# Kernel tuning notes

Measured on AMD Instinct MI355X. Metric: run time of the kernel, lower is better.

Reference implementation:

```python
import jax, jax.numpy as jnp
import numpy as np

B, C, D, H, W = 1, 128, 8, 32, 32
NH, HD = 8, 16            # num_heads, head_dim = C // NH
PD, PH, PW = 2, 4, 4      # local patch dims
RD, RH, RW = 2, 2, 2      # global K/V reduction ratios
MLPH = 4 * C              # mlp_ratio = 4
EPS = 1e-5
SCALE = HD ** -0.5


def setup_inputs() -> dict:
    key = jax.random.key(0)
    ks = iter(jax.random.split(key, 16))
    def w(shape, scale=0.02):
        return jax.random.normal(next(ks), shape, jnp.float32) * scale
    inp = {"x": jax.random.normal(next(ks), (B, C, D, H, W), jnp.float32)}
    for p in ("l", "g"):  # local branch / global branch transformer blocks
        inp[f"{p}_n1_g"] = jnp.ones((C,), jnp.float32)
        inp[f"{p}_n1_b"] = jnp.zeros((C,), jnp.float32)
        inp[f"{p}_qkv_w"] = w((3 * C, C))            # Linear(dim, 3*dim, bias=False)
        inp[f"{p}_proj_w"] = w((C, C))
        inp[f"{p}_proj_b"] = jnp.zeros((C,), jnp.float32)
        inp[f"{p}_n2_g"] = jnp.ones((C,), jnp.float32)
        inp[f"{p}_n2_b"] = jnp.zeros((C,), jnp.float32)
        inp[f"{p}_fc1_w"] = w((MLPH, C))
        inp[f"{p}_fc1_b"] = jnp.zeros((MLPH,), jnp.float32)
        inp[f"{p}_fc2_w"] = w((C, MLPH))
        inp[f"{p}_fc2_b"] = jnp.zeros((C,), jnp.float32)
    inp["g_ke_w"] = w((C, C, RD, RH, RW))  # Conv3d(dim, dim, k=stride=(2,2,2), bias=False)
    inp["g_ve_w"] = w((C, C, RD, RH, RW))
    inp["g_nk_g"] = jnp.ones((HD,), jnp.float32)
    inp["g_nk_b"] = jnp.zeros((HD,), jnp.float32)
    inp["g_nv_g"] = jnp.ones((HD,), jnp.float32)
    inp["g_nv_b"] = jnp.zeros((HD,), jnp.float32)
    return inp


def _ln(t, g, b):
    m = t.mean(-1, keepdims=True)
    v = jnp.square(t - m).mean(-1, keepdims=True)
    return (t - m) * jax.lax.rsqrt(v + EPS) * g + b


def _mlp(t, w1, b1, w2, b2):
    return jax.nn.gelu(t @ w1.T + b1, approximate=False) @ w2.T + b2


def _forward(x, l_n1_g, l_n1_b, l_qkv_w, l_proj_w, l_proj_b, l_n2_g, l_n2_b,
             l_fc1_w, l_fc1_b, l_fc2_w, l_fc2_b,
             g_n1_g, g_n1_b, g_qkv_w, g_ke_w, g_ve_w, g_nk_g, g_nk_b,
             g_nv_g, g_nv_b, g_proj_w, g_proj_b, g_n2_g, g_n2_b,
             g_fc1_w, g_fc1_b, g_fc2_w, g_fc2_b):
    nd, nh, nw = D // PD, H // PH, W // PW
    R, Npl = nd * nh * nw, PD * PH * PW
    N = D * H * W

    # ---------------- Local branch ----------------
    # (B,C,D,H,W) -> (B, R, Npl, C) patch tokens
    loc = x.reshape(B, C, nd, PD, nh, PH, nw, PW)
    loc = loc.transpose(0, 2, 4, 6, 3, 5, 7, 1).reshape(B, R, Npl, C)
    y = _ln(loc, l_n1_g, l_n1_b)
    qkv = (y @ l_qkv_w.T).reshape(B, R, Npl, 3, NH, HD).transpose(3, 0, 1, 4, 2, 5)
    q, k, v = qkv[0], qkv[1], qkv[2]  # (B,R,NH,Npl,HD)
    attn = jax.nn.softmax(jnp.einsum('brhnd,brhmd->brhnm', q, k) * SCALE, axis=-1)
    o = jnp.einsum('brhnm,brhmd->brhnd', attn, v)
    # faithful to torch: (attn@v).transpose(-1,-2).reshape(B,R,Npl,C)
    o = jnp.swapaxes(o, -1, -2).reshape(B, R, Npl, C)
    loc = loc + (o @ l_proj_w.T + l_proj_b)
    loc = loc + _mlp(_ln(loc, l_n2_g, l_n2_b), l_fc1_w, l_fc1_b, l_fc2_w, l_fc2_b)
    # back to (B,C,D,H,W)
    loc_y = loc.reshape(B, nd, nh, nw, PD, PH, PW, C)
    loc_y = loc_y.transpose(0, 7, 1, 4, 2, 5, 3, 6).reshape(B, C, D, H, W)

    # ---------------- Global branch ----------------
    g = x.reshape(B, C, N).transpose(0, 2, 1)  # (B,N,C)
    y = _ln(g, g_n1_g, g_n1_b)
    qkv = y @ g_qkv_w.T  # (B,N,3C)
    q, k, v = jnp.split(qkv, 3, axis=-1)
    qh = q.reshape(B, N, NH, HD).transpose(0, 2, 1, 3)  # (B,NH,N,HD)
    dn = ('NCDHW', 'OIDHW', 'NCDHW')
    def _reduce(t, wc):
        tm = t.transpose(0, 2, 1).reshape(B, C, D, H, W)
        tr = jax.lax.conv_general_dilated(tm, wc, (RD, RH, RW), 'VALID',
                                          dimension_numbers=dn)
        nr = tr.shape[2] * tr.shape[3] * tr.shape[4]
        return tr.reshape(B, C, nr).transpose(0, 2, 1).reshape(B, nr, NH, HD).transpose(0, 2, 1, 3)
    kr = _ln(_reduce(k, g_ke_w), g_nk_g, g_nk_b)  # (B,NH,Nr,HD)
    vr = _ln(_reduce(v, g_ve_w), g_nv_g, g_nv_b)
    attn = jax.nn.softmax(jnp.einsum('bhnd,bhmd->bhnm', qh, kr) * SCALE, axis=-1)
    o = jnp.einsum('bhnm,bhmd->bhnd', attn, vr)
    o = o.transpose(0, 2, 1, 3).reshape(B, N, C)
    g = g + (o @ g_proj_w.T + g_proj_b)
    g = g + _mlp(_ln(g, g_n2_g, g_n2_b), g_fc1_w, g_fc1_b, g_fc2_w, g_fc2_b)
    glo_y = g.transpose(0, 2, 1).reshape(B, C, D, H, W)

    # ---------------- Gate ----------------
    return x * jax.nn.sigmoid(loc_y + glo_y)


def reference(x, l_n1_g, l_n1_b, l_qkv_w, l_proj_w, l_proj_b, l_n2_g, l_n2_b,
              l_fc1_w, l_fc1_b, l_fc2_w, l_fc2_b,
              g_n1_g, g_n1_b, g_qkv_w, g_ke_w, g_ve_w, g_nk_g, g_nk_b,
              g_nv_g, g_nv_b, g_proj_w, g_proj_b, g_n2_g, g_n2_b,
              g_fc1_w, g_fc1_b, g_fc2_w, g_fc2_b):
    return _forward(x, l_n1_g, l_n1_b, l_qkv_w, l_proj_w, l_proj_b, l_n2_g, l_n2_b,
                    l_fc1_w, l_fc1_b, l_fc2_w, l_fc2_b,
                    g_n1_g, g_n1_b, g_qkv_w, g_ke_w, g_ve_w, g_nk_g, g_nk_b,
                    g_nv_g, g_nv_b, g_proj_w, g_proj_b, g_n2_g, g_n2_b,
                    g_fc1_w, g_fc1_b, g_fc2_w, g_fc2_b)
```

## Files before the change

### kernel.cpp

```cpp
#include <hip/hip_runtime.h>
#include <math.h>

#define N_TOK 8192
#define C_DIM 128
#define NHD   8
#define HDIM  16
#define NR    1024
#define EPSV  1e-5f
#define QK_SCALE 0.25f
#define QK_L2E  0.36067376f

typedef __attribute__((ext_vector_type(8))) short short8;
typedef __attribute__((ext_vector_type(4))) float f32x4;

__device__ __forceinline__ float gelu_f(float v) {
    return 0.5f * v * (1.0f + erff(v * 0.70710678118654752f));
}
__device__ __forceinline__ float uaf(unsigned int u) {
    union { unsigned int u; float f; } x; x.u = u; return x.f;
}
__device__ __forceinline__ short f2b(float v) {
    union { float f; unsigned int u; } x; x.f = v;
    unsigned int r = x.u + 0x7fffu + ((x.u >> 16) & 1u);
    return (short)(r >> 16);
}
__device__ __forceinline__ unsigned int pk2(float a, float b) {
    return (unsigned int)(unsigned short)f2b(a) | ((unsigned int)(unsigned short)f2b(b) << 16);
}
__device__ __forceinline__ void ld16bf(const short* p, float* d) {
    uint4 a = *(const uint4*)p;
    uint4 b = *(const uint4*)(p + 8);
    d[0]  = uaf(a.x << 16); d[1]  = uaf(a.x & 0xffff0000u);
    d[2]  = uaf(a.y << 16); d[3]  = uaf(a.y & 0xffff0000u);
    d[4]  = uaf(a.z << 16); d[5]  = uaf(a.z & 0xffff0000u);
    d[6]  = uaf(a.w << 16); d[7]  = uaf(a.w & 0xffff0000u);
    d[8]  = uaf(b.x << 16); d[9]  = uaf(b.x & 0xffff0000u);
    d[10] = uaf(b.y << 16); d[11] = uaf(b.y & 0xffff0000u);
    d[12] = uaf(b.z << 16); d[13] = uaf(b.z & 0xffff0000u);
    d[14] = uaf(b.w << 16); d[15] = uaf(b.w & 0xffff0000u);
}

struct CvtDesc { const float* src; short* dst; int n; int pad; };
struct CvtArgs { CvtDesc d[10]; };

__global__ __launch_bounds__(256) void prep_k(const float* __restrict__ x,
                                              const float* __restrict__ g1, const float* __restrict__ b1,
                                              const float* __restrict__ g2, const float* __restrict__ b2,
                                              float* __restrict__ xt,
                                              short* __restrict__ o1, short* __restrict__ o2,
                                              CvtArgs ca) {
    __shared__ float tile[32][132];
    int t = threadIdx.x;
    if (blockIdx.x >= 256) {
        int bid = blockIdx.x - 256;
#pragma unroll 1
        for (int d = 0; d < 10; ++d) {
            CvtDesc dd = ca.d[d];
            if (dd.pad) {
                for (int i = bid * 256 + t; i < dd.n; i += 40 * 256) {
                    int co = i >> 10, qq = i & 1023;
                    dd.dst[co * 1024 + ((qq & 7) << 7) + (qq >> 3)] = f2b(dd.src[i]);
                }
            } else {
                for (int i = bid * 256 + t; i < dd.n; i += 40 * 256)
                    dd.dst[i] = f2b(dd.src[i]);
            }
        }
        return;
    }
    int n0 = blockIdx.x * 32;
#pragma unroll
    for (int k = 0; k < 16; ++k) {
        int f = t + k * 256;
        int n = f & 31, c = f >> 5;
        tile[n][c] = x[(size_t)c * N_TOK + n0 + n];
    }
    __syncthreads();
    int tk = t >> 3, cb = (t & 7) * 16;
    float v[16];
    float s = 0.f, sq = 0.f;
#pragma unroll
    for (int i = 0; i < 16; ++i) {
        v[i] = tile[tk][cb + i];
        s += v[i]; sq += v[i] * v[i];
    }
    s += __shfl_xor(s, 1);  s += __shfl_xor(s, 2);  s += __shfl_xor(s, 4);
    sq += __shfl_xor(sq, 1); sq += __shfl_xor(sq, 2); sq += __shfl_xor(sq, 4);
    float m = s * (1.0f / 128.0f);
    float var = sq * (1.0f / 128.0f) - m * m;
    float rs = rsqrtf(var + EPSV);
    int tok = n0 + tk;
    float* xp = xt + (size_t)tok * C_DIM + cb;
    *(float4*)(xp)      = make_float4(v[0], v[1], v[2], v[3]);
    *(float4*)(xp + 4)  = make_float4(v[4], v[5], v[6], v[7]);
    *(float4*)(xp + 8)  = make_float4(v[8], v[9], v[10], v[11]);
    *(float4*)(xp + 12) = make_float4(v[12], v[13], v[14], v[15]);
    float hA[16], hB[16];
#pragma unroll
    for (int i = 0; i < 16; ++i) {
        float hn = (v[i] - m) * rs;
        hA[i] = hn * g1[cb + i] + b1[cb + i];
        hB[i] = hn * g2[cb + i] + b2[cb + i];
    }
    uint4 ua0 = {pk2(hA[0], hA[1]), pk2(hA[2], hA[3]), pk2(hA[4], hA[5]), pk2(hA[6], hA[7])};
    uint4 ua1 = {pk2(hA[8], hA[9]), pk2(hA[10], hA[11]), pk2(hA[12], hA[13]), pk2(hA[14], hA[15])};
    uint4 ub0 = {pk2(hB[0], hB[1]), pk2(hB[2], hB[3]), pk2(hB[4], hB[5]), pk2(hB[6], hB[7])};
    uint4 ub1 = {pk2(hB[8], hB[9]), pk2(hB[10], hB[11]), pk2(hB[12], hB[13]), pk2(hB[14], hB[15])};
    *(uint4*)(o1 + (size_t)tok * C_DIM + cb)     = ua0;
    *(uint4*)(o1 + (size_t)tok * C_DIM + cb + 8) = ua1;
    *(uint4*)(o2 + (size_t)tok * C_DIM + cb)     = ub0;
    *(uint4*)(o2 + (size_t)tok * C_DIM + cb + 8) = ub1;
}

__global__ __launch_bounds__(256) void ln2_pair_k(const float* __restrict__ in0,
                                                  const float* __restrict__ g0, const float* __restrict__ b0,
                                                  short* __restrict__ o0,
                                                  const float* __restrict__ in1,
                                                  const float* __restrict__ g1, const float* __restrict__ b1,
                                                  short* __restrict__ o1) {
    int blk = blockIdx.x;
    bool sel = blk >= 2048;
    blk &= 2047;
    const float* in = sel ? in1 : in0;
    const float* g  = sel ? g1 : g0;
    const float* b  = sel ? b1 : b0;
    short* o        = sel ? o1 : o0;
    int lane = threadIdx.x & 63;
    int n = blk * 4 + (threadIdx.x >> 6);
    float v0 = in[(size_t)n * C_DIM + lane];
    float v1 = in[(size_t)n * C_DIM + 64 + lane];
    float s = v0 + v1, sq = v0 * v0 + v1 * v1;
#pragma unroll
    for (int off = 32; off >= 1; off >>= 1) {
        s += __shfl_xor(s, off);
        sq += __shfl_xor(sq, off);
    }
    float m = s * (1.0f / 128.0f);
    float var = sq * (1.0f / 128.0f) - m * m;
    float rs = rsqrtf(var + EPSV);
    o[(size_t)n * C_DIM + lane]      = f2b((v0 - m) * rs * g[lane] + b[lane]);
    o[(size_t)n * C_DIM + 64 + lane] = f2b((v1 - m) * rs * g[lane + 64] + b[lane + 64]);
}

struct MArgs {
    const short* A[2]; const short* W[2];
    const float* bias[2]; const float* res[2];
    void* out[2];
};
template <int EPI>
__global__ __launch_bounds__(256) void mgemm_k(MArgs ga, int M, int N, int K) {
    int zi = blockIdx.z;
    const short* A = ga.A[zi];
    const short* W = ga.W[zi];
    __shared__ short As[128 * 64];
    __shared__ short Bs[128 * 64];
    int t = threadIdx.x;
    int w = t >> 6, l = t & 63;
    int m0 = blockIdx.x * 128, n0 = blockIdx.y * 128;
    int wm = (w >> 1) * 64, wn = (w & 1) * 64;

    f32x4 acc[4][4];
#pragma unroll
    for (int a = 0; a < 4; ++a)
#pragma unroll
        for (int b = 0; b < 4; ++b) acc[a][b] = f32x4{0.f, 0.f, 0.f, 0.f};

    for (int k0 = 0; k0 < K; k0 += 64) {
        __syncthreads();
#pragma unroll
        for (int c = 0; c < 4; ++c) {
            int chunk = c * 256 + t;
            int row = chunk >> 3;
            int slot = chunk & 7;
            int ss = slot ^ (row & 7);
            uint4 av = *(const uint4*)(A + (size_t)(m0 + row) * K + k0 + slot * 8);
            *(uint4*)(As + row * 64 + ss * 8) = av;
            uint4 wv = *(const uint4*)(W + (size_t)(n0 + row) * K + k0 + slot * 8);
            *(uint4*)(Bs + row * 64 + ss * 8) = wv;
        }
        __syncthreads();
#pragma unroll
        for (int kk = 0; kk < 2; ++kk) {
            short8 af[4], bf[4];
            int sl = kk * 4 + (l >> 4);
#pragma unroll
            for (int mf = 0; mf < 4; ++mf) {
                int row = wm + mf * 16 + (l & 15);
                af[mf] = *(const short8*)(As + row * 64 + (sl ^ (row & 7)) * 8);
            }
#pragma unroll
            for (int nf = 0; nf < 4; ++nf) {
                int row = wn + nf * 16 + (l & 15);
                bf[nf] = *(const short8*)(Bs + row * 64 + (sl ^ (row & 7)) * 8);
            }
#pragma unroll
            for (int mf = 0; mf < 4; ++mf)
#pragma unroll
                for (int nf = 0; nf < 4; ++nf)
                    acc[mf][nf] = __builtin_amdgcn_mfma_f32_16x16x32_bf16(
                        af[mf], bf[nf], acc[mf][nf], 0, 0, 0);
        }
    }

#pragma unroll
    for (int mf = 0; mf < 4; ++mf) {
#pragma unroll
        for (int nf = 0; nf < 4; ++nf) {
            int col = n0 + wn + nf * 16 + (l & 15);
#pragma unroll
            for (int j = 0; j < 4; ++j) {
                int row = m0 + wm + mf * 16 + (l >> 4) * 4 + j;
                float v = acc[mf][nf][j];
                if (EPI == 0) {
                    ((short*)ga.out[zi])[(size_t)row * N + col] = f2b(v);
                } else if (EPI == 1) {
                    v += ga.bias[zi][col] + ga.res[zi][(size_t)row * N + col];
                    ((float*)ga.out[zi])[(size_t)row * N + col] = v;
                } else if (EPI == 2) {
                    v = gelu_f(v + ga.bias[zi][col]);
                    ((short*)ga.out[zi])[(size_t)row * N + col] = f2b(v);
                }
            }
        }
    }
}

struct CLArgs {
    const short* qkv_g; const short* wk; const short* wv;
    float* kpart; float* vpart;
    const short* qkv_l; short* ob;
};
__global__ __launch_bounds__(256) void convlat_k(CLArgs ga) {
    __shared__ char smem[32768];
    int t = threadIdx.x;
    if (blockIdx.x < 128) {
        int bid = blockIdx.x;
        int m0 = (bid & 7) * 128;
        int zi = bid >> 6;
        int slice = (bid >> 3) & 7;
        const short* Abase = ga.qkv_g + (zi ? 256 : 128);
        const short* W = zi ? ga.wv : ga.wk;
        float* outp = zi ? ga.vpart : ga.kpart;
        short* As = (short*)smem;
        short* Bs = (short*)smem + 128 * 64;
        int w = t >> 6, l = t & 63;
        int wm = (w >> 1) * 64, wn = (w & 1) * 64;
        int kbeg = slice * 128;

        f32x4 acc[4][4];
#pragma unroll
        for (int a = 0; a < 4; ++a)
#pragma unroll
            for (int b = 0; b < 4; ++b) acc[a][b] = f32x4{0.f, 0.f, 0.f, 0.f};

        for (int k0 = kbeg; k0 < kbeg + 128; k0 += 64) {
            __syncthreads();
            int off = k0 >> 7;
            int od = off >> 2, oh = (off >> 1) & 1, ow = off & 1;
#pragma unroll
            for (int c = 0; c < 4; ++c) {
                int chunk = c * 256 + t;
                int row = chunk >> 3;
                int slot = chunk & 7;
                int ss = slot ^ (row & 7);
                int nr = m0 + row;
                int ci = (k0 & 127) + slot * 8;
                int n = (2 * (nr >> 8) + od) * 1024 + (2 * ((nr >> 4) & 15) + oh) * 32
                        + 2 * (nr & 15) + ow;
                uint4 av = *(const uint4*)(Abase + (size_t)n * 384 + ci);
                *(uint4*)(As + row * 64 + ss * 8) = av;
                uint4 wv2 = *(const uint4*)(W + (size_t)row * 1024 + k0 + slot * 8);
                *(uint4*)(Bs + row * 64 + ss * 8) = wv2;
            }
            __syncthreads();
#pragma unroll
            for (int kk = 0; kk < 2; ++kk) {
                short8 af[4], bf[4];
                int sl = kk * 4 + (l >> 4);
#pragma unroll
                for (int mf = 0; mf < 4; ++mf) {
                    int row = wm + mf * 16 + (l & 15);
                    af[mf] = *(const short8*)(As + row * 64 + (sl ^ (row & 7)) * 8);
                }
#pragma unroll
                for (int nf = 0; nf < 4; ++nf) {
                    int row = wn + nf * 16 + (l & 15);
                    bf[nf] = *(const short8*)(Bs + row * 64 + (sl ^ (row & 7)) * 8);
                }
#pragma unroll
                for (int mf = 0; mf < 4; ++mf)
#pragma unroll
                    for (int nf = 0; nf < 4; ++nf)
                        acc[mf][nf] = __builtin_amdgcn_mfma_f32_16x16x32_bf16(
                            af[mf], bf[nf], acc[mf][nf], 0, 0, 0);
            }
        }
#pragma unroll
        for (int mf = 0; mf < 4; ++mf)
#pragma unroll
            for (int nf = 0; nf < 4; ++nf) {
                int col = wn + nf * 16 + (l & 15);
#pragma unroll
                for (int j = 0; j < 4; ++j) {
                    int row = m0 + wm + mf * 16 + (l >> 4) * 4 + j;
                    outp[(size_t)slice * (NR * C_DIM) + (size_t)row * C_DIM + col] =
                        acc[mf][nf][j];
                }
            }
        return;
    }
    float (*ks)[32][HDIM] = (float(*)[32][HDIM])smem;
    float (*vs)[32][HDIM] = (float(*)[32][HDIM])(smem + 16384);
    int m = t & 31, h = t >> 5, r = blockIdx.x - 128;
    int zd = r >> 6, zh = (r >> 3) & 7, zw = r & 7;
    int pd = m >> 4, ph = (m >> 2) & 3, pw = m & 3;
    int n = (zd * 2 + pd) * 1024 + (zh * 4 + ph) * 32 + (zw * 4 + pw);
    const short* base = ga.qkv_l + (size_t)n * 384 + h * HDIM;
    float q[16], kt[16], vt[16];
    ld16bf(base, q);
    ld16bf(base + 128, kt);
    ld16bf(base + 256, vt);
#pragma unroll
    for (int d = 0; d < 16; ++d) { ks[h][m][d] = kt[d]; vs[h][m][d] = vt[d]; }
    __syncthreads();
    float s[32];
#pragma unroll
    for (int j = 0; j < 32; ++j) {
        float d = 0.f;
#pragma unroll
        for (int dd = 0; dd < 16; ++dd) d += q[dd] * ks[h][j][dd];
        s[j] = __expf(d * QK_SCALE);
    }
    float sum = 0.f;
#pragma unroll
    for (int j = 0; j < 32; ++j) sum += s[j];
    float inv = 1.0f / sum;
    float oo[16] = {};
#pragma unroll
    for (int j = 0; j < 32; ++j) {
        float p = s[j] * inv;
#pragma unroll
        for (int dd = 0; dd < 16; ++dd) oo[dd] += p * vs[h][j][dd];
    }
#pragma unroll
    for (int dd = 0; dd < 16; ++dd) {
        int n2 = h * 4 + (dd >> 2);
        int c2 = (dd & 3) * 32 + m;
        int pd2 = n2 >> 4, ph2 = (n2 >> 2) & 3, pw2 = n2 & 3;
        int nn = (zd * 2 + pd2) * 1024 + (zh * 4 + ph2) * 32 + (zw * 4 + pw2);
        ga.ob[(size_t)nn * C_DIM + c2] = f2b(oo[dd]);
    }
}

__global__ __launch_bounds__(256) void ln_head_sum_k(const float* __restrict__ kpart,
                                                     const float* __restrict__ vpart,
                                                     const float* __restrict__ gk, const float* __restrict__ bk,
                                                     const float* __restrict__ gv, const float* __restrict__ bv,
                                                     short* __restrict__ kout, short* __restrict__ vout) {
    int idx = blockIdx.x * 256 + threadIdx.x;
    bool sel = idx >= 8192;
    int id2 = idx & 8191;
    const float* part = sel ? vpart : kpart;
    const float* g    = sel ? gv : gk;
    const float* b    = sel ? bv : bk;
    int nr = id2 >> 3, h = id2 & 7;
    size_t base = (size_t)nr * C_DIM + h * HDIM;
    float v[16] = {};
#pragma unroll
    for (int p = 0; p < 8; ++p) {
        const float* pp = part + (size_t)p * (NR * C_DIM) + base;
#pragma unroll
        for (int d4 = 0; d4 < 4; ++d4) {
            float4 t = *(const float4*)(pp + d4 * 4);
            v[d4 * 4 + 0] += t.x; v[d4 * 4 + 1] += t.y;
            v[d4 * 4 + 2] += t.z; v[d4 * 4 + 3] += t.w;
        }
    }
    float s = 0.f;
#pragma unroll
    for (int i = 0; i < 16; ++i) s += v[i];
    float m = s * (1.0f / 16.0f);
    float sq = 0.f;
#pragma unroll
    for (int i = 0; i < 16; ++i) { float d = v[i] - m; sq += d * d; }
    float rs = rsqrtf(sq * (1.0f / 16.0f) + EPSV);
    if (!sel) {
        short* op = kout + (size_t)h * (NR * HDIM) + (size_t)nr * HDIM;
#pragma unroll
        for (int i = 0; i < 16; ++i)
            op[i] = f2b(((v[i] - m) * rs * g[i] + b[i]) * QK_L2E);
    } else {
        short* op = vout + (size_t)h * (HDIM * NR) + nr;
#pragma unroll
        for (int i = 0; i < 16; ++i)
            op[(size_t)i * NR] = f2b((v[i] - m) * rs * g[i] + b[i]);
    }
}

__global__ __launch_bounds__(512) void gattn_k(const short* __restrict__ qkv,
                                               const short* __restrict__ kb,
                                               const short* __restrict__ vt,
                                               short* __restrict__ ob) {
    __shared__ short plds[8][2048];
    __shared__ float comb[4][64][5];
    int t = threadIdx.x;
    int w = t >> 6, l = t & 63;
    int h = blockIdx.y;
    int lr = l & 15, lq = l >> 4;
    int qw = w & 3, kw = w >> 2;
    int q0 = blockIdx.x * 64 + qw * 16;

    short8 qf = short8{0, 0, 0, 0, 0, 0, 0, 0};
    if (lq < 2)
        qf = *(const short8*)(qkv + (size_t)(q0 + lr) * 384 + h * HDIM + lq * 8);

    const short* kh = kb + (size_t)h * (NR * HDIM);
    const short* vh = vt + (size_t)h * (HDIM * NR);
    short* pw = &plds[w][0];

    const f32x4 zz = {0.f, 0.f, 0.f, 0.f};
    f32x4 oacc = {0.f, 0.f, 0.f, 0.f};
    float rs = 0.f;

    for (int c = 0; c < 4; ++c) {
        int kbase = kw * 512 + c * 128;
        f32x4 s[8];
#pragma unroll
        for (int nf = 0; nf < 8; ++nf) {
            short8 kf = short8{0, 0, 0, 0, 0, 0, 0, 0};
            if (lq < 2)
                kf = *(const short8*)(kh + (size_t)(kbase + nf * 16 + lr) * HDIM + lq * 8);
            s[nf] = __builtin_amdgcn_mfma_f32_16x16x32_bf16(kf, qf, zz, 0, 0, 0);
        }
#pragma unroll
        for (int nf = 0; nf < 8; ++nf) {
            float p0 = exp2f(s[nf][0]);
            float p1 = exp2f(s[nf][1]);
            float p2 = exp2f(s[nf][2]);
            float p3 = exp2f(s[nf][3]);
            rs += (p0 + p1) + (p2 + p3);
            unsigned int u01, u23;
            asm("v_cvt_pk_bf16_f32 %0, %1, %2" : "=v"(u01) : "v"(p0), "v"(p1));
            asm("v_cvt_pk_bf16_f32 %0, %1, %2" : "=v"(u23) : "v"(p2), "v"(p3));
            int k0 = nf * 16 + lq * 4;
            int sw = (lr & 7) << 3;
            *(unsigned int*)&pw[lr * 128 + (k0 ^ sw)]       = u01;
            *(unsigned int*)&pw[lr * 128 + ((k0 + 2) ^ sw)] = u23;
        }
#pragma unroll
        for (int ks = 0; ks < 4; ++ks) {
            short8 pf = *(const short8*)&pw[(lr * 128 + ks * 32 + lq * 8) ^ ((lr & 7) << 3)];
            short8 vf = *(const short8*)(vh + (size_t)lr * NR + kbase + ks * 32 + lq * 8);
            oacc = __builtin_amdgcn_mfma_f32_16x16x32_bf16(pf, vf, oacc, 0, 0, 0);
        }
    }
    rs += __shfl_xor(rs, 16);
    rs += __shfl_xor(rs, 32);
    if (w >= 4) {
        comb[w - 4][l][0] = oacc[0];
        comb[w - 4][l][1] = oacc[1];
        comb[w - 4][l][2] = oacc[2];
        comb[w - 4][l][3] = oacc[3];
        comb[w - 4][l][4] = rs;
    }
    __syncthreads();
    if (w < 4) {
        oacc[0] += comb[w][l][0];
        oacc[1] += comb[w][l][1];
        oacc[2] += comb[w][l][2];
        oacc[3] += comb[w][l][3];
        rs += comb[w][l][4];
        float r0 = __shfl(rs, lq * 4 + 0);
        float r1 = __shfl(rs, lq * 4 + 1);
        float r2 = __shfl(rs, lq * 4 + 2);
        float r3 = __shfl(rs, lq * 4 + 3);
        size_t base_o = (size_t)(q0 + lq * 4) * C_DIM + h * HDIM + lr;
        ob[base_o]             = f2b(oacc[0] / r0);
        ob[base_o + C_DIM]     = f2b(oacc[1] / r1);
        ob[base_o + 2 * C_DIM] = f2b(oacc[2] / r2);
        ob[base_o + 3 * C_DIM] = f2b(oacc[3] / r3);
    }
}

__global__ __launch_bounds__(256) void gate_k(const float* __restrict__ x,
                                              const float* __restrict__ lf, const float* __restrict__ gf,
                                              float* __restrict__ out) {
    __shared__ float tile[32][33];
    int n0 = blockIdx.x * 32, c0 = blockIdx.y * 32;
    int tx = threadIdx.x, ty = threadIdx.y;
#pragma unroll
    for (int k = 0; k < 4; ++k) {
        int n = n0 + ty + k * 8, c = c0 + tx;
        tile[ty + k * 8][tx] = lf[(size_t)n * C_DIM + c] + gf[(size_t)n * C_DIM + c];
    }
    __syncthreads();
#pragma unroll
    for (int k = 0; k < 4; ++k) {
        int c = c0 + ty + k * 8, n = n0 + tx;
        float z = tile[tx][ty + k * 8];
        float sg = 1.0f / (1.0f + __expf(-z));
        out[(size_t)c * N_TOK + n] = x[(size_t)c * N_TOK + n] * sg;
    }
}

extern "C" void kernel_launch(void* const* d_in, const int* in_sizes, int n_in,
                              void* d_out, int out_size, void* d_ws, size_t ws_size,
                              hipStream_t stream) {
    const float* x        = (const float*)d_in[0];
    const float* l_n1_g   = (const float*)d_in[1];
    const float* l_n1_b   = (const float*)d_in[2];
    const float* l_qkv_w  = (const float*)d_in[3];
    const float* l_proj_w = (const float*)d_in[4];
    const float* l_proj_b = (const float*)d_in[5];
    const float* l_n2_g   = (const float*)d_in[6];
    const float* l_n2_b   = (const float*)d_in[7];
    const float* l_fc1_w  = (const float*)d_in[8];
    const float* l_fc1_b  = (const float*)d_in[9];
    const float* l_fc2_w  = (const float*)d_in[10];
    const float* l_fc2_b  = (const float*)d_in[11];
    const float* g_n1_g   = (const float*)d_in[12];
    const float* g_n1_b   = (const float*)d_in[13];
    const float* g_qkv_w  = (const float*)d_in[14];
    const float* g_proj_w = (const float*)d_in[15];
    const float* g_proj_b = (const float*)d_in[16];
    const float* g_n2_g   = (const float*)d_in[17];
    const float* g_n2_b   = (const float*)d_in[18];
    const float* g_fc1_w  = (const float*)d_in[19];
    const float* g_fc1_b  = (const float*)d_in[20];
    const float* g_fc2_w  = (const float*)d_in[21];
    const float* g_fc2_b  = (const float*)d_in[22];
    const float* g_ke_w   = (const float*)d_in[23];
    const float* g_ve_w   = (const float*)d_in[24];
    const float* g_nk_g   = (const float*)d_in[25];
    const float* g_nk_b   = (const float*)d_in[26];
    const float* g_nv_g   = (const float*)d_in[27];
    const float* g_nv_b   = (const float*)d_in[28];
    float* out = (float*)d_out;

    char* base = (char*)d_ws;
    float* xt     = (float*)(base);
    float* t1_l   = (float*)(base + (4ull  << 20));
    float* t1_g   = (float*)(base + (8ull  << 20));
    short* yA16   = (short*)(base + (12ull << 20));
    short* yG16   = (short*)(base + (14ull << 20));
    short* t2_l   = yA16;
    short* t2_g   = yG16;
    float* locfin = (float*)(base + (12ull << 20));
    short* obuf_l = (short*)(base + (16ull << 20));
    short* obuf_g = (short*)(base + (18ull << 20));
    float* glofin = (float*)(base + (16ull << 20));
    short* qkv_l  = (short*)(base + (20ull << 20));
    short* qkv_g  = (short*)(base + (26ull << 20));
    short* h1_l   = (short*)(base + (32ull << 20));
    float* kpart  = (float*)(base + (32ull << 20));
    float* vpart  = (float*)(base + (36ull << 20));
    short* h1_g   = (short*)(base + (40ull << 20));
    short* kb16   = (short*)(base + (48ull << 20));
    short* vt16   = (short*)(base + (48ull << 20) + (512ull << 10));
    short* wts    = (short*)(base + (49ull << 20));

    const int L_QKV = 0,      L_PROJ = 49152, L_FC1 = 65536,  L_FC2 = 131072;
    const int G_QKV = 196608, G_PROJ = 245760, G_FC1 = 262144, G_FC2 = 327680;
    const int G_KE  = 393216, G_VE   = 524288;

    CvtArgs ca;
    ca.d[0] = {l_qkv_w,  wts + L_QKV,  49152, 0};
    ca.d[1] = {l_proj_w, wts + L_PROJ, 16384, 0};
    ca.d[2] = {l_fc1_w,  wts + L_FC1,  65536, 0};
    ca.d[3] = {l_fc2_w,  wts + L_FC2,  65536, 0};
    ca.d[4] = {g_qkv_w,  wts + G_QKV,  49152, 0};
    ca.d[5] = {g_proj_w, wts + G_PROJ, 16384, 0};
    ca.d[6] = {g_fc1_w,  wts + G_FC1,  65536, 0};
    ca.d[7] = {g_fc2_w,  wts + G_FC2,  65536, 0};
    ca.d[8] = {g_ke_w,   wts + G_KE,  131072, 1};
    ca.d[9] = {g_ve_w,   wts + G_VE,  131072, 1};

    prep_k<<<296, 256, 0, stream>>>(x, l_n1_g, l_n1_b, g_n1_g, g_n1_b, xt, yA16, yG16, ca);

    MArgs a_qkv = {{yA16, yG16}, {wts + L_QKV, wts + G_QKV}, {nullptr, nullptr}, {nullptr, nullptr}, {qkv_l, qkv_g}};
    mgemm_k<0><<<dim3(64, 3, 2), 256, 0, stream>>>(a_qkv, N_TOK, 384, 128);

    CLArgs cla = {qkv_g, wts + G_KE, wts + G_VE, kpart, vpart, qkv_l, obuf_l};
    convlat_k<<<384, 256, 0, stream>>>(cla);

    ln_head_sum_k<<<64, 256, 0, stream>>>(kpart, vpart, g_nk_g, g_nk_b, g_nv_g, g_nv_b, kb16, vt16);

    gattn_k<<<dim3(128, 8), 512, 0, stream>>>(qkv_g, kb16, vt16, obuf_g);

    MArgs a_pj = {{obuf_l, obuf_g}, {wts + L_PROJ, wts + G_PROJ}, {l_proj_b, g_proj_b}, {xt, xt}, {t1_l, t1_g}};
    mgemm_k<1><<<dim3(64, 1, 2), 256, 0, stream>>>(a_pj, N_TOK, 128, 128);

    ln2_pair_k<<<4096, 256, 0, stream>>>(t1_l, l_n2_g, l_n2_b, t2_l, t1_g, g_n2_g, g_n2_b, t2_g);

    MArgs a_f1 = {{t2_l, t2_g}, {wts + L_FC1, wts + G_FC1}, {l_fc1_b, g_fc1_b}, {nullptr, nullptr}, {h1_l, h1_g}};
    mgemm_k<2><<<dim3(64, 4, 2), 256, 0, stream>>>(a_f1, N_TOK, 512, 128);

    MArgs a_f2 = {{h1_l, h1_g}, {wts + L_FC2, wts + G_FC2}, {l_fc2_b, g_fc2_b}, {t1_l, t1_g}, {locfin, glofin}};
    mgemm_k<1><<<dim3(64, 1, 2), 256, 0, stream>>>(a_f2, N_TOK, 128, 512);

    gate_k<<<dim3(256, 4), dim3(32, 8), 0, stream>>>(x, locfin, glofin, out);
}
```

Baseline: 140.7 us.

## Double-buffer GEMM tiles with direct global-to-LDS loads, tanh GELU, coalesced V stores

```diff
diff --git a/kernel.cpp b/kernel.cpp
--- a/kernel.cpp
+++ b/kernel.cpp
@@ -14,7 +14,9 @@
 typedef __attribute__((ext_vector_type(4))) float f32x4;
 
 __device__ __forceinline__ float gelu_f(float v) {
-    return 0.5f * v * (1.0f + erff(v * 0.70710678118654752f));
+    float u = 0.7978845608f * (v + 0.044715f * v * v * v);
+    float e = exp2f(2.885390082f * u);
+    return v * (e / (e + 1.0f));
 }
 __device__ __forceinline__ float uaf(unsigned int u) {
     union { unsigned int u; float f; } x; x.u = u; return x.f;
@@ -38,6 +40,12 @@
     d[10] = uaf(b.y << 16); d[11] = uaf(b.y & 0xffff0000u);
     d[12] = uaf(b.z << 16); d[13] = uaf(b.z & 0xffff0000u);
     d[14] = uaf(b.w << 16); d[15] = uaf(b.w & 0xffff0000u);
+}
+
+__device__ __forceinline__ void gload16(const void* g, void* l) {
+    __builtin_amdgcn_global_load_lds(
+        (const __attribute__((address_space(1))) unsigned int*)g,
+        (__attribute__((address_space(3))) unsigned int*)l, 16, 0, 0);
 }
 
 struct CvtDesc { const float* src; short* dst; int n; int pad; };
@@ -152,8 +160,8 @@
     int zi = blockIdx.z;
     const short* A = ga.A[zi];
     const short* W = ga.W[zi];
-    __shared__ short As[128 * 64];
-    __shared__ short Bs[128 * 64];
+    __shared__ short As[2][128 * 64];
+    __shared__ short Bs[2][128 * 64];
     int t = threadIdx.x;
     int w = t >> 6, l = t & 63;
     int m0 = blockIdx.x * 128, n0 = blockIdx.y * 128;
@@ -165,20 +173,29 @@
 #pragma unroll
         for (int b = 0; b < 4; ++b) acc[a][b] = f32x4{0.f, 0.f, 0.f, 0.f};
 
-    for (int k0 = 0; k0 < K; k0 += 64) {
-        __syncthreads();
+    auto STAGE = [&](int buf, int k0) {
 #pragma unroll
         for (int c = 0; c < 4; ++c) {
-            int chunk = c * 256 + t;
-            int row = chunk >> 3;
-            int slot = chunk & 7;
-            int ss = slot ^ (row & 7);
-            uint4 av = *(const uint4*)(A + (size_t)(m0 + row) * K + k0 + slot * 8);
-            *(uint4*)(As + row * 64 + ss * 8) = av;
-            uint4 wv = *(const uint4*)(W + (size_t)(n0 + row) * K + k0 + slot * 8);
-            *(uint4*)(Bs + row * 64 + ss * 8) = wv;
-        }
-        __syncthreads();
+            int g0 = c * 256 + w * 64;
+            int g  = g0 + l;
+            int row = g >> 3, ss = g & 7;
+            int slot = ss ^ (row & 7);
+            gload16(A + (size_t)(m0 + row) * K + k0 + slot * 8, &As[buf][g0 * 8]);
+            gload16(W + (size_t)(n0 + row) * K + k0 + slot * 8, &Bs[buf][g0 * 8]);
+        }
+    };
+
+    int NT = K >> 6;
+    STAGE(0, 0);
+    int cur = 0;
+    for (int it = 0; it < NT; ++it) {
+        if (it + 1 < NT) {
+            STAGE(cur ^ 1, (it + 1) << 6);
+            asm volatile("s_waitcnt vmcnt(8)" ::: "memory");
+        } else {
+            asm volatile("s_waitcnt vmcnt(0)" ::: "memory");
+        }
+        __builtin_amdgcn_s_barrier();
 #pragma unroll
         for (int kk = 0; kk < 2; ++kk) {
             short8 af[4], bf[4];
@@ -186,12 +203,12 @@
 #pragma unroll
             for (int mf = 0; mf < 4; ++mf) {
                 int row = wm + mf * 16 + (l & 15);
-                af[mf] = *(const short8*)(As + row * 64 + (sl ^ (row & 7)) * 8);
+                af[mf] = *(const short8*)(&As[cur][row * 64 + (sl ^ (row & 7)) * 8]);
             }
 #pragma unroll
             for (int nf = 0; nf < 4; ++nf) {
                 int row = wn + nf * 16 + (l & 15);
-                bf[nf] = *(const short8*)(Bs + row * 64 + (sl ^ (row & 7)) * 8);
+                bf[nf] = *(const short8*)(&Bs[cur][row * 64 + (sl ^ (row & 7)) * 8]);
             }
 #pragma unroll
             for (int mf = 0; mf < 4; ++mf)
@@ -200,6 +217,10 @@
                     acc[mf][nf] = __builtin_amdgcn_mfma_f32_16x16x32_bf16(
                         af[mf], bf[nf], acc[mf][nf], 0, 0, 0);
         }
+        asm volatile("s_waitcnt lgkmcnt(0)" ::: "memory");
+        __builtin_amdgcn_sched_barrier(0);
+        __builtin_amdgcn_s_barrier();
+        cur ^= 1;
     }
 
 #pragma unroll
@@ -231,7 +252,7 @@
     const short* qkv_l; short* ob;
 };
 __global__ __launch_bounds__(256) void convlat_k(CLArgs ga) {
-    __shared__ char smem[32768];
+    __shared__ char smem[65536];
     int t = threadIdx.x;
     if (blockIdx.x < 128) {
         int bid = blockIdx.x;
@@ -241,11 +262,12 @@
         const short* Abase = ga.qkv_g + (zi ? 256 : 128);
         const short* W = zi ? ga.wv : ga.wk;
         float* outp = zi ? ga.vpart : ga.kpart;
-        short* As = (short*)smem;
-        short* Bs = (short*)smem + 128 * 64;
+        short (*As)[8192] = (short(*)[8192])smem;
+        short (*Bs)[8192] = (short(*)[8192])(smem + 32768);
         int w = t >> 6, l = t & 63;
         int wm = (w >> 1) * 64, wn = (w & 1) * 64;
         int kbeg = slice * 128;
+        int od = slice >> 2, oh = (slice >> 1) & 1, ow = slice & 1;
 
         f32x4 acc[4][4];
 #pragma unroll
@@ -253,26 +275,31 @@
 #pragma unroll
             for (int b = 0; b < 4; ++b) acc[a][b] = f32x4{0.f, 0.f, 0.f, 0.f};
 
-        for (int k0 = kbeg; k0 < kbeg + 128; k0 += 64) {
-            __syncthreads();
-            int off = k0 >> 7;
-            int od = off >> 2, oh = (off >> 1) & 1, ow = off & 1;
+        auto STAGE = [&](int buf, int k0) {
 #pragma unroll
             for (int c = 0; c < 4; ++c) {
-                int chunk = c * 256 + t;
-                int row = chunk >> 3;
-                int slot = chunk & 7;
-                int ss = slot ^ (row & 7);
+                int g0 = c * 256 + w * 64;
+                int g  = g0 + l;
+                int row = g >> 3, ss = g & 7;
+                int slot = ss ^ (row & 7);
                 int nr = m0 + row;
-                int ci = (k0 & 127) + slot * 8;
                 int n = (2 * (nr >> 8) + od) * 1024 + (2 * ((nr >> 4) & 15) + oh) * 32
                         + 2 * (nr & 15) + ow;
-                uint4 av = *(const uint4*)(Abase + (size_t)n * 384 + ci);
-                *(uint4*)(As + row * 64 + ss * 8) = av;
-                uint4 wv2 = *(const uint4*)(W + (size_t)row * 1024 + k0 + slot * 8);
-                *(uint4*)(Bs + row * 64 + ss * 8) = wv2;
-            }
-            __syncthreads();
+                gload16(Abase + (size_t)n * 384 + (k0 & 127) + slot * 8, &As[buf][g0 * 8]);
+                gload16(W + (size_t)row * 1024 + k0 + slot * 8, &Bs[buf][g0 * 8]);
+            }
+        };
+
+        STAGE(0, kbeg);
+        int cur = 0;
+        for (int it = 0; it < 2; ++it) {
+            if (it == 0) {
+                STAGE(1, kbeg + 64);
+                asm volatile("s_waitcnt vmcnt(8)" ::: "memory");
+            } else {
+                asm volatile("s_waitcnt vmcnt(0)" ::: "memory");
+            }
+            __builtin_amdgcn_s_barrier();
 #pragma unroll
             for (int kk = 0; kk < 2; ++kk) {
                 short8 af[4], bf[4];
@@ -280,12 +307,12 @@
 #pragma unroll
                 for (int mf = 0; mf < 4; ++mf) {
                     int row = wm + mf * 16 + (l & 15);
-                    af[mf] = *(const short8*)(As + row * 64 + (sl ^ (row & 7)) * 8);
+                    af[mf] = *(const short8*)(&As[cur][row * 64 + (sl ^ (row & 7)) * 8]);
                 }
 #pragma unroll
                 for (int nf = 0; nf < 4; ++nf) {
                     int row = wn + nf * 16 + (l & 15);
-                    bf[nf] = *(const short8*)(Bs + row * 64 + (sl ^ (row & 7)) * 8);
+                    bf[nf] = *(const short8*)(&Bs[cur][row * 64 + (sl ^ (row & 7)) * 8]);
                 }
 #pragma unroll
                 for (int mf = 0; mf < 4; ++mf)
@@ -294,6 +321,10 @@
                         acc[mf][nf] = __builtin_amdgcn_mfma_f32_16x16x32_bf16(
                             af[mf], bf[nf], acc[mf][nf], 0, 0, 0);
             }
+            asm volatile("s_waitcnt lgkmcnt(0)" ::: "memory");
+            __builtin_amdgcn_sched_barrier(0);
+            __builtin_amdgcn_s_barrier();
+            cur ^= 1;
         }
 #pragma unroll
         for (int mf = 0; mf < 4; ++mf)
@@ -357,12 +388,14 @@
                                                      const float* __restrict__ gk, const float* __restrict__ bk,
                                                      const float* __restrict__ gv, const float* __restrict__ bv,
                                                      short* __restrict__ kout, short* __restrict__ vout) {
-    int idx = blockIdx.x * 256 + threadIdx.x;
-    bool sel = idx >= 8192;
-    int id2 = idx & 8191;
+    __shared__ float vlds[8][16][33];
+    int t = threadIdx.x;
+    bool sel = blockIdx.x >= 32;
+    int b = sel ? (blockIdx.x - 32) : blockIdx.x;
+    int id2 = b * 256 + t;
     const float* part = sel ? vpart : kpart;
     const float* g    = sel ? gv : gk;
-    const float* b    = sel ? bv : bk;
+    const float* bb   = sel ? bv : bk;
     int nr = id2 >> 3, h = id2 & 7;
     size_t base = (size_t)nr * C_DIM + h * HDIM;
     float v[16] = {};
@@ -371,9 +404,9 @@
         const float* pp = part + (size_t)p * (NR * C_DIM) + base;
 #pragma unroll
         for (int d4 = 0; d4 < 4; ++d4) {
-            float4 t = *(const float4*)(pp + d4 * 4);
-            v[d4 * 4 + 0] += t.x; v[d4 * 4 + 1] += t.y;
-            v[d4 * 4 + 2] += t.z; v[d4 * 4 + 3] += t.w;
+            float4 tv = *(const float4*)(pp + d4 * 4);
+            v[d4 * 4 + 0] += tv.x; v[d4 * 4 + 1] += tv.y;
+            v[d4 * 4 + 2] += tv.z; v[d4 * 4 + 3] += tv.w;
         }
     }
     float s = 0.f;
@@ -388,13 +421,22 @@
         short* op = kout + (size_t)h * (NR * HDIM) + (size_t)nr * HDIM;
 #pragma unroll
         for (int i = 0; i < 16; ++i)
-            op[i] = f2b(((v[i] - m) * rs * g[i] + b[i]) * QK_L2E);
-    } else {
-        short* op = vout + (size_t)h * (HDIM * NR) + nr;
-#pragma unroll
-        for (int i = 0; i < 16; ++i)
-            op[(size_t)i * NR] = f2b((v[i] - m) * rs * g[i] + b[i]);
-    }
+            op[i] = f2b(((v[i] - m) * rs * g[i] + bb[i]) * QK_L2E);
+        return;
+    }
+    int nr_l = t >> 3;
+#pragma unroll
+    for (int i = 0; i < 16; ++i)
+        vlds[h][i][nr_l] = (v[i] - m) * rs * g[i] + bb[i];
+    __syncthreads();
+    int row = t >> 1, half = t & 1;
+    int h2 = row >> 4, i2 = row & 15;
+    const float* src = &vlds[h2][i2][half * 16];
+    uint4 u0 = {pk2(src[0], src[1]), pk2(src[2], src[3]), pk2(src[4], src[5]), pk2(src[6], src[7])};
+    uint4 u1 = {pk2(src[8], src[9]), pk2(src[10], src[11]), pk2(src[12], src[13]), pk2(src[14], src[15])};
+    short* dst = vout + (size_t)h2 * (HDIM * NR) + (size_t)i2 * NR + b * 32 + half * 16;
+    *(uint4*)(dst)     = u0;
+    *(uint4*)(dst + 8) = u1;
 }
 
 __global__ __launch_bounds__(512) void gattn_k(const short* __restrict__ qkv,
```

Result: faster. 137.9 us (median of 2 runs) (-2.0%).
